# Optimization experiments

Measured on AMD Instinct MI355X. Metric: run time of the kernel, lower is better.

## Reference

```python
import jax, jax.numpy as jnp
import numpy as np

N_NODES = 40000
N_EDGES = 640000
IN_CH, HID_CH, OUT_CH = 128, 128, 64


def setup_inputs() -> dict:
    key = jax.random.key(0)
    ks = jax.random.split(key, 8)
    x = jax.random.normal(ks[0], (N_NODES, IN_CH), dtype=jnp.float32)
    edge_index = jax.random.randint(ks[1], (2, N_EDGES), 0, N_NODES, dtype=jnp.int32)
    s = 1.0 / np.sqrt(IN_CH)
    W1_rel = jax.random.normal(ks[2], (HID_CH, IN_CH), dtype=jnp.float32) * s
    W1_root = jax.random.normal(ks[3], (HID_CH, IN_CH), dtype=jnp.float32) * s
    b1 = jnp.zeros((HID_CH,), dtype=jnp.float32)
    s2 = 1.0 / np.sqrt(HID_CH)
    W2_rel = jax.random.normal(ks[4], (OUT_CH, HID_CH), dtype=jnp.float32) * s2
    W2_root = jax.random.normal(ks[5], (OUT_CH, HID_CH), dtype=jnp.float32) * s2
    b2 = jnp.zeros((OUT_CH,), dtype=jnp.float32)
    return {"x": x, "edge_index": edge_index, "W1_rel": W1_rel, "W1_root": W1_root,
            "b1": b1, "W2_rel": W2_rel, "W2_root": W2_root, "b2": b2}


def graph_conv(x, edge_index, W_rel, W_root, b):
    # PyG GraphConv (aggr='add'): out_i = W_rel @ (sum_{j->i} x_j) + W_root @ x_i + b
    src, dst = edge_index[0], edge_index[1]
    agg = jax.ops.segment_sum(x[src], dst, num_segments=x.shape[0])  # [N, d_in]
    return agg @ W_rel.T + x @ W_root.T + b


def reference(x, edge_index, W1_rel, W1_root, b1, W2_rel, W2_root, b2):
    h = jax.nn.relu(graph_conv(x, edge_index, W1_rel, W1_root, b1))
    return graph_conv(h, edge_index, W2_rel, W2_root, b2)
```

## Files before the change

### kernel.cpp

```cpp
#include <hip/hip_runtime.h>

#define N_NODES 40000
#define N_EDGES 640000

typedef __attribute__((ext_vector_type(8))) short short8;
typedef __attribute__((ext_vector_type(4))) float f32x4;

__device__ __forceinline__ float b2f_hi(uint v) {
  uint u = v & 0xffff0000u;
  return __builtin_bit_cast(float, u);
}
__device__ __forceinline__ float b2f_lo(uint v) {
  uint u = v << 16;
  return __builtin_bit_cast(float, u);
}
__device__ __forceinline__ ushort f2b(float f) {
  uint u = __builtin_bit_cast(uint, f);
  u += 0x7fffu + ((u >> 16) & 1u);
  return (ushort)(u >> 16);
}

__global__ __launch_bounds__(256) void k_count(
    const int* __restrict__ ei, int* __restrict__ deg) {
  int e = blockIdx.x * 256 + threadIdx.x;
  atomicAdd(&deg[ei[N_EDGES + e]], 1);
}

__global__ __launch_bounds__(256) void k_scanA(
    const int* __restrict__ deg, int* __restrict__ local,
    int* __restrict__ bsum) {
  const int t = threadIdx.x;
  const int base = blockIdx.x * 1024 + t * 4;
  int v0 = 0, v1 = 0, v2 = 0, v3 = 0;
  if (base < N_NODES) {
    int4 v = *reinterpret_cast<const int4*>(deg + base);
    v0 = v.x; v1 = v.y; v2 = v.z; v3 = v.w;
  }
  const int tot = v0 + v1 + v2 + v3;
  const int lane = t & 63;
  int ws = tot;
#pragma unroll
  for (int off = 1; off < 64; off <<= 1) {
    int y = __shfl_up(ws, off, 64);
    if (lane >= off) ws += y;
  }
  __shared__ int wsum[4];
  if (lane == 63) wsum[t >> 6] = ws;
  __syncthreads();
  const int w = t >> 6;
  int wbase = 0;
#pragma unroll
  for (int i = 0; i < 4; ++i) wbase += (i < w) ? wsum[i] : 0;
  const int incl = wbase + ws;
  const int excl = incl - tot;
  if (base < N_NODES) {
    int4 o;
    o.x = excl;
    o.y = excl + v0;
    o.z = excl + v0 + v1;
    o.w = excl + v0 + v1 + v2;
    *reinterpret_cast<int4*>(local + base) = o;
  }
  if (t == 255) bsum[blockIdx.x] = incl;
}

__global__ __launch_bounds__(64) void k_scanB(
    const int* __restrict__ bsum, int* __restrict__ bbase) {
  const int t = threadIdx.x;
  int v = (t < 40) ? bsum[t] : 0;
  int ws = v;
#pragma unroll
  for (int off = 1; off < 64; off <<= 1) {
    int y = __shfl_up(ws, off, 64);
    if (t >= off) ws += y;
  }
  if (t < 40) bbase[t] = ws - v;
}

__global__ __launch_bounds__(256) void k_scanC(
    const int* __restrict__ local, const int* __restrict__ bbase,
    int* __restrict__ offs, int* __restrict__ cursor) {
  int i = blockIdx.x * 256 + threadIdx.x;
  if (i < N_NODES) {
    int v = local[i] + bbase[i >> 10];
    offs[i] = v;
    cursor[i] = v;
  }
  if (i == 0) offs[N_NODES] = N_EDGES;
}

__global__ __launch_bounds__(256) void k_fill(
    const int* __restrict__ ei, int* __restrict__ cursor,
    int* __restrict__ csr_src) {
  int e = blockIdx.x * 256 + threadIdx.x;
  int dst = ei[N_EDGES + e];
  int idx = atomicAdd(&cursor[dst], 1);
  csr_src[idx] = ei[e];
}

__global__ __launch_bounds__(256) void k_cvt_x(
    const float* __restrict__ x, ushort* __restrict__ xb) {
  const int i = (blockIdx.x * 256 + threadIdx.x) * 8;
  float4 v0 = *reinterpret_cast<const float4*>(x + i);
  float4 v1 = *reinterpret_cast<const float4*>(x + i + 4);
  uint4 o;
  o.x = (uint)f2b(v0.x) | ((uint)f2b(v0.y) << 16);
  o.y = (uint)f2b(v0.z) | ((uint)f2b(v0.w) << 16);
  o.z = (uint)f2b(v1.x) | ((uint)f2b(v1.y) << 16);
  o.w = (uint)f2b(v1.z) | ((uint)f2b(v1.w) << 16);
  *reinterpret_cast<uint4*>(xb + i) = o;
}

__global__ __launch_bounds__(256) void k_cvt_w(
    const float* __restrict__ W1rel, const float* __restrict__ W1root,
    const float* __restrict__ W2rel, const float* __restrict__ W2root,
    ushort* __restrict__ Wb1, ushort* __restrict__ Wb2) {
  const int i = (blockIdx.x * 256 + threadIdx.x) * 4;
  const float* src;
  ushort* dst;
  if (i < 32768) {
    dst = Wb1 + i;
    src = (i < 16384) ? (W1rel + i) : (W1root + (i - 16384));
  } else {
    int j = i - 32768;
    dst = Wb2 + j;
    src = (j < 8192) ? (W2rel + j) : (W2root + (j - 8192));
  }
  float4 v = *reinterpret_cast<const float4*>(src);
  uint2 o;
  o.x = (uint)f2b(v.x) | ((uint)f2b(v.y) << 16);
  o.y = (uint)f2b(v.z) | ((uint)f2b(v.w) << 16);
  *reinterpret_cast<uint2*>(dst) = o;
}

template <int NCT, bool F32OUT1>
__global__ __launch_bounds__(256) void k_gemm_mfma(
    const ushort* __restrict__ A, const ushort* __restrict__ Wb,
    const float* __restrict__ bias, ushort* __restrict__ out0,
    void* __restrict__ out1v) {
  constexpr int HC = NCT * 8;
  const int t = threadIdx.x;
  const int lane = t & 63;
  const int n0 = blockIdx.x * 64 + (t >> 6) * 16;
  const int lr = lane & 15;
  const int hk = (lane >> 4) * 8;

  const ushort* arow = A + (size_t)(n0 + lr) * 128 + hk;
  const short8 a0 = *reinterpret_cast<const short8*>(arow);
  const short8 a1 = *reinterpret_cast<const short8*>(arow + 32);
  const short8 a2 = *reinterpret_cast<const short8*>(arow + 64);
  const short8 a3 = *reinterpret_cast<const short8*>(arow + 96);

  const int orow = n0 + (lane >> 4) * 4;

#pragma unroll
  for (int ct = 0; ct < NCT; ++ct) {
    const ushort* wrow = Wb + (size_t)(ct * 16 + lr) * 128 + hk;
    f32x4 acc = {0.f, 0.f, 0.f, 0.f};
    acc = __builtin_amdgcn_mfma_f32_16x16x32_bf16(
        a0, *reinterpret_cast<const short8*>(wrow), acc, 0, 0, 0);
    acc = __builtin_amdgcn_mfma_f32_16x16x32_bf16(
        a1, *reinterpret_cast<const short8*>(wrow + 32), acc, 0, 0, 0);
    acc = __builtin_amdgcn_mfma_f32_16x16x32_bf16(
        a2, *reinterpret_cast<const short8*>(wrow + 64), acc, 0, 0, 0);
    acc = __builtin_amdgcn_mfma_f32_16x16x32_bf16(
        a3, *reinterpret_cast<const short8*>(wrow + 96), acc, 0, 0, 0);

    if (ct < NCT / 2) {
      const int col = ct * 16 + lr;
#pragma unroll
      for (int i = 0; i < 4; ++i)
        out0[(size_t)(orow + i) * HC + col] = f2b(acc[i]);
    } else {
      const int col = (ct - NCT / 2) * 16 + lr;
      const float bb = bias[col];
      if (F32OUT1) {
        float* o1 = (float*)out1v;
#pragma unroll
        for (int i = 0; i < 4; ++i)
          o1[(size_t)(orow + i) * HC + col] = acc[i] + bb;
      } else {
        ushort* o1 = (ushort*)out1v;
#pragma unroll
        for (int i = 0; i < 4; ++i)
          o1[(size_t)(orow + i) * HC + col] = f2b(acc[i] + bb);
      }
    }
  }
}

__global__ __launch_bounds__(256) void k_gather_relu(
    const ushort* __restrict__ xr, ushort* __restrict__ h,
    const int* __restrict__ csr_src, const int* __restrict__ offs) {
  int n = blockIdx.x * 4 + (threadIdx.x >> 6);
  n = __builtin_amdgcn_readfirstlane(n);
  const int lane = threadIdx.x & 63;
  const int s = offs[n], e = offs[n + 1];
  float s00 = 0.f, s01 = 0.f, s10 = 0.f, s11 = 0.f;
  float s20 = 0.f, s21 = 0.f, s30 = 0.f, s31 = 0.f;
  int i = s;
  for (; i + 3 < e; i += 4) {
    int e0 = csr_src[i], e1 = csr_src[i + 1];
    int e2 = csr_src[i + 2], e3 = csr_src[i + 3];
    uint v0 = *reinterpret_cast<const uint*>(xr + (size_t)e0 * 128 + lane * 2);
    uint v1 = *reinterpret_cast<const uint*>(xr + (size_t)e1 * 128 + lane * 2);
    uint v2 = *reinterpret_cast<const uint*>(xr + (size_t)e2 * 128 + lane * 2);
    uint v3 = *reinterpret_cast<const uint*>(xr + (size_t)e3 * 128 + lane * 2);
    s00 += b2f_lo(v0); s01 += b2f_hi(v0);
    s10 += b2f_lo(v1); s11 += b2f_hi(v1);
    s20 += b2f_lo(v2); s21 += b2f_hi(v2);
    s30 += b2f_lo(v3); s31 += b2f_hi(v3);
  }
  for (; i < e; ++i) {
    uint v = *reinterpret_cast<const uint*>(
        xr + (size_t)csr_src[i] * 128 + lane * 2);
    s00 += b2f_lo(v); s01 += b2f_hi(v);
  }
  const float g0 = (s00 + s10) + (s20 + s30);
  const float g1 = (s01 + s11) + (s21 + s31);
  ushort* hp = h + (size_t)n * 128 + lane * 2;
  uint xov = *reinterpret_cast<const uint*>(hp);
  float r0 = fmaxf(b2f_lo(xov) + g0, 0.f);
  float r1 = fmaxf(b2f_hi(xov) + g1, 0.f);
  *reinterpret_cast<uint*>(hp) = (uint)f2b(r0) | ((uint)f2b(r1) << 16);
}

__global__ __launch_bounds__(256) void k_gather64(
    const ushort* __restrict__ t2, const int* __restrict__ csr_src,
    const int* __restrict__ offs, float* __restrict__ out) {
  int n = blockIdx.x * 4 + (threadIdx.x >> 6);
  n = __builtin_amdgcn_readfirstlane(n);
  const int lane = threadIdx.x & 63;
  const int s = offs[n], e = offs[n + 1];
  float a0 = 0.f, a1 = 0.f, a2 = 0.f, a3 = 0.f;
  int i = s;
  for (; i + 3 < e; i += 4) {
    int e0 = csr_src[i], e1 = csr_src[i + 1];
    int e2 = csr_src[i + 2], e3 = csr_src[i + 3];
    a0 += b2f_lo((uint)t2[(size_t)e0 * 64 + lane]);
    a1 += b2f_lo((uint)t2[(size_t)e1 * 64 + lane]);
    a2 += b2f_lo((uint)t2[(size_t)e2 * 64 + lane]);
    a3 += b2f_lo((uint)t2[(size_t)e3 * 64 + lane]);
  }
  for (; i < e; ++i)
    a0 += b2f_lo((uint)t2[(size_t)csr_src[i] * 64 + lane]);
  out[(size_t)n * 64 + lane] += (a0 + a1) + (a2 + a3);
}

extern "C" void kernel_launch(void* const* d_in, const int* in_sizes, int n_in,
                              void* d_out, int out_size, void* d_ws, size_t ws_size,
                              hipStream_t stream) {
  const float* x = (const float*)d_in[0];
  const int* ei = (const int*)d_in[1];
  const float* W1rel = (const float*)d_in[2];
  const float* W1root = (const float*)d_in[3];
  const float* b1 = (const float*)d_in[4];
  const float* W2rel = (const float*)d_in[5];
  const float* W2root = (const float*)d_in[6];
  const float* b2 = (const float*)d_in[7];
  float* out = (float*)d_out;

  ushort* xb = (ushort*)d_ws;
  ushort* xr = xb + (size_t)N_NODES * 128;
  ushort* xo = xr + (size_t)N_NODES * 128;
  ushort* t2 = xo + (size_t)N_NODES * 128;
  ushort* Wb1 = t2 + (size_t)N_NODES * 64;
  ushort* Wb2 = Wb1 + 32768;
  int* deg = (int*)(Wb2 + 16384);
  int* offs = deg + N_NODES;
  int* cursor = offs + (N_NODES + 1);
  int* csr_src = cursor + N_NODES;
  int* bsum = csr_src + N_EDGES;
  int* bbase = bsum + 64;
  int* local = (int*)xr;

  k_cvt_x<<<(N_NODES * 128 / 8) / 256, 256, 0, stream>>>(x, xb);
  k_cvt_w<<<48, 256, 0, stream>>>(W1rel, W1root, W2rel, W2root, Wb1, Wb2);

  hipMemsetAsync(deg, 0, (size_t)N_NODES * sizeof(int), stream);
  k_count<<<N_EDGES / 256, 256, 0, stream>>>(ei, deg);
  k_scanA<<<(N_NODES + 1023) / 1024, 256, 0, stream>>>(deg, local, bsum);
  k_scanB<<<1, 64, 0, stream>>>(bsum, bbase);
  k_scanC<<<(N_NODES + 255) / 256, 256, 0, stream>>>(local, bbase, offs, cursor);
  k_fill<<<N_EDGES / 256, 256, 0, stream>>>(ei, cursor, csr_src);

  k_gemm_mfma<16, false><<<N_NODES / 64, 256, 0, stream>>>(
      xb, Wb1, b1, xr, (void*)xo);
  k_gather_relu<<<N_NODES / 4, 256, 0, stream>>>(xr, xo, csr_src, offs);

  k_gemm_mfma<8, true><<<N_NODES / 64, 256, 0, stream>>>(
      xo, Wb2, b2, t2, (void*)out);
  k_gather64<<<N_NODES / 4, 256, 0, stream>>>(t2, csr_src, offs, out);
}
```

Baseline: 240.2 us.

## Fuse layer-1 gather/ReLU into layer-2 GEMM and fold x conversion into GEMM1

```diff
diff --git a/kernel.cpp b/kernel.cpp
--- a/kernel.cpp
+++ b/kernel.cpp
@@ -18,6 +18,35 @@
   uint u = __builtin_bit_cast(uint, f);
   u += 0x7fffu + ((u >> 16) & 1u);
   return (ushort)(u >> 16);
+}
+
+__global__ __launch_bounds__(256) void k_prep(
+    const float* __restrict__ W1rel, const float* __restrict__ W1root,
+    const float* __restrict__ W2rel, const float* __restrict__ W2root,
+    ushort* __restrict__ Wb1, ushort* __restrict__ Wb2,
+    int* __restrict__ deg) {
+  const int b = blockIdx.x;
+  if (b < 48) {
+    const int i = (b * 256 + threadIdx.x) * 4;
+    const float* src;
+    ushort* dst;
+    if (i < 32768) {
+      dst = Wb1 + i;
+      src = (i < 16384) ? (W1rel + i) : (W1root + (i - 16384));
+    } else {
+      int j = i - 32768;
+      dst = Wb2 + j;
+      src = (j < 8192) ? (W2rel + j) : (W2root + (j - 8192));
+    }
+    float4 v = *reinterpret_cast<const float4*>(src);
+    uint2 o;
+    o.x = (uint)f2b(v.x) | ((uint)f2b(v.y) << 16);
+    o.y = (uint)f2b(v.z) | ((uint)f2b(v.w) << 16);
+    *reinterpret_cast<uint2*>(dst) = o;
+  } else {
+    const int i = (b - 48) * 256 + threadIdx.x;
+    if (i < N_NODES) deg[i] = 0;
+  }
 }
 
 __global__ __launch_bounds__(256) void k_count(
@@ -98,66 +127,117 @@
   csr_src[idx] = ei[e];
 }
 
-__global__ __launch_bounds__(256) void k_cvt_x(
-    const float* __restrict__ x, ushort* __restrict__ xb) {
-  const int i = (blockIdx.x * 256 + threadIdx.x) * 8;
-  float4 v0 = *reinterpret_cast<const float4*>(x + i);
-  float4 v1 = *reinterpret_cast<const float4*>(x + i + 4);
-  uint4 o;
-  o.x = (uint)f2b(v0.x) | ((uint)f2b(v0.y) << 16);
-  o.y = (uint)f2b(v0.z) | ((uint)f2b(v0.w) << 16);
-  o.z = (uint)f2b(v1.x) | ((uint)f2b(v1.y) << 16);
-  o.w = (uint)f2b(v1.z) | ((uint)f2b(v1.w) << 16);
-  *reinterpret_cast<uint4*>(xb + i) = o;
-}
-
-__global__ __launch_bounds__(256) void k_cvt_w(
-    const float* __restrict__ W1rel, const float* __restrict__ W1root,
-    const float* __restrict__ W2rel, const float* __restrict__ W2root,
-    ushort* __restrict__ Wb1, ushort* __restrict__ Wb2) {
-  const int i = (blockIdx.x * 256 + threadIdx.x) * 4;
-  const float* src;
-  ushort* dst;
-  if (i < 32768) {
-    dst = Wb1 + i;
-    src = (i < 16384) ? (W1rel + i) : (W1root + (i - 16384));
-  } else {
-    int j = i - 32768;
-    dst = Wb2 + j;
-    src = (j < 8192) ? (W2rel + j) : (W2root + (j - 8192));
-  }
-  float4 v = *reinterpret_cast<const float4*>(src);
-  uint2 o;
-  o.x = (uint)f2b(v.x) | ((uint)f2b(v.y) << 16);
-  o.y = (uint)f2b(v.z) | ((uint)f2b(v.w) << 16);
-  *reinterpret_cast<uint2*>(dst) = o;
-}
-
-template <int NCT, bool F32OUT1>
-__global__ __launch_bounds__(256) void k_gemm_mfma(
-    const ushort* __restrict__ A, const ushort* __restrict__ Wb,
-    const float* __restrict__ bias, ushort* __restrict__ out0,
-    void* __restrict__ out1v) {
-  constexpr int HC = NCT * 8;
+__global__ __launch_bounds__(256) void k_gemm1_mfma(
+    const float* __restrict__ x, const ushort* __restrict__ Wb1,
+    const float* __restrict__ b1, ushort* __restrict__ xr,
+    ushort* __restrict__ xo) {
   const int t = threadIdx.x;
   const int lane = t & 63;
   const int n0 = blockIdx.x * 64 + (t >> 6) * 16;
   const int lr = lane & 15;
   const int hk = (lane >> 4) * 8;
 
-  const ushort* arow = A + (size_t)(n0 + lr) * 128 + hk;
-  const short8 a0 = *reinterpret_cast<const short8*>(arow);
-  const short8 a1 = *reinterpret_cast<const short8*>(arow + 32);
-  const short8 a2 = *reinterpret_cast<const short8*>(arow + 64);
-  const short8 a3 = *reinterpret_cast<const short8*>(arow + 96);
+  const float* arow = x + (size_t)(n0 + lr) * 128 + hk;
+  short8 a[4];
+#pragma unroll
+  for (int c = 0; c < 4; ++c) {
+    float4 f0 = *reinterpret_cast<const float4*>(arow + c * 32);
+    float4 f1 = *reinterpret_cast<const float4*>(arow + c * 32 + 4);
+    short8 v;
+    v[0] = (short)f2b(f0.x); v[1] = (short)f2b(f0.y);
+    v[2] = (short)f2b(f0.z); v[3] = (short)f2b(f0.w);
+    v[4] = (short)f2b(f1.x); v[5] = (short)f2b(f1.y);
+    v[6] = (short)f2b(f1.z); v[7] = (short)f2b(f1.w);
+    a[c] = v;
+  }
 
   const int orow = n0 + (lane >> 4) * 4;
 
 #pragma unroll
-  for (int ct = 0; ct < NCT; ++ct) {
-    const ushort* wrow = Wb + (size_t)(ct * 16 + lr) * 128 + hk;
+  for (int ct = 0; ct < 16; ++ct) {
+    const ushort* wrow = Wb1 + (size_t)(ct * 16 + lr) * 128 + hk;
     f32x4 acc = {0.f, 0.f, 0.f, 0.f};
     acc = __builtin_amdgcn_mfma_f32_16x16x32_bf16(
+        a[0], *reinterpret_cast<const short8*>(wrow), acc, 0, 0, 0);
+    acc = __builtin_amdgcn_mfma_f32_16x16x32_bf16(
+        a[1], *reinterpret_cast<const short8*>(wrow + 32), acc, 0, 0, 0);
+    acc = __builtin_amdgcn_mfma_f32_16x16x32_bf16(
+        a[2], *reinterpret_cast<const short8*>(wrow + 64), acc, 0, 0, 0);
+    acc = __builtin_amdgcn_mfma_f32_16x16x32_bf16(
+        a[3], *reinterpret_cast<const short8*>(wrow + 96), acc, 0, 0, 0);
+
+    if (ct < 8) {
+      const int col = ct * 16 + lr;
+#pragma unroll
+      for (int i = 0; i < 4; ++i)
+        xr[(size_t)(orow + i) * 128 + col] = f2b(acc[i]);
+    } else {
+      const int col = (ct - 8) * 16 + lr;
+      const float bb = b1[col];
+#pragma unroll
+      for (int i = 0; i < 4; ++i)
+        xo[(size_t)(orow + i) * 128 + col] = f2b(acc[i] + bb);
+    }
+  }
+}
+
+__global__ __launch_bounds__(256) void k_gemm2_fused(
+    const ushort* __restrict__ xr, const ushort* __restrict__ xo,
+    const ushort* __restrict__ Wb2, const float* __restrict__ b2,
+    const int* __restrict__ csr_src, const int* __restrict__ offs,
+    ushort* __restrict__ t2, float* __restrict__ out) {
+  __shared__ ushort sH[64][136];
+  const int t = threadIdx.x;
+  const int wave = t >> 6;
+  const int lane = t & 63;
+  const int nb = blockIdx.x * 64 + wave * 16;
+
+  for (int r = 0; r < 16; ++r) {
+    const int n = nb + r;
+    const int s = offs[n], e = offs[n + 1];
+    float s00 = 0.f, s01 = 0.f, s10 = 0.f, s11 = 0.f;
+    float s20 = 0.f, s21 = 0.f, s30 = 0.f, s31 = 0.f;
+    int i = s;
+    for (; i + 3 < e; i += 4) {
+      int e0 = csr_src[i], e1 = csr_src[i + 1];
+      int e2 = csr_src[i + 2], e3 = csr_src[i + 3];
+      uint v0 = *reinterpret_cast<const uint*>(xr + (size_t)e0 * 128 + lane * 2);
+      uint v1 = *reinterpret_cast<const uint*>(xr + (size_t)e1 * 128 + lane * 2);
+      uint v2 = *reinterpret_cast<const uint*>(xr + (size_t)e2 * 128 + lane * 2);
+      uint v3 = *reinterpret_cast<const uint*>(xr + (size_t)e3 * 128 + lane * 2);
+      s00 += b2f_lo(v0); s01 += b2f_hi(v0);
+      s10 += b2f_lo(v1); s11 += b2f_hi(v1);
+      s20 += b2f_lo(v2); s21 += b2f_hi(v2);
+      s30 += b2f_lo(v3); s31 += b2f_hi(v3);
+    }
+    for (; i < e; ++i) {
+      uint v = *reinterpret_cast<const uint*>(
+          xr + (size_t)csr_src[i] * 128 + lane * 2);
+      s00 += b2f_lo(v); s01 += b2f_hi(v);
+    }
+    uint xov = *reinterpret_cast<const uint*>(xo + (size_t)n * 128 + lane * 2);
+    float r0 = fmaxf(b2f_lo(xov) + ((s00 + s10) + (s20 + s30)), 0.f);
+    float r1 = fmaxf(b2f_hi(xov) + ((s01 + s11) + (s21 + s31)), 0.f);
+    *reinterpret_cast<uint*>(&sH[wave * 16 + r][lane * 2]) =
+        (uint)f2b(r0) | ((uint)f2b(r1) << 16);
+  }
+  __syncthreads();
+
+  const int lr = lane & 15;
+  const int hk = (lane >> 4) * 8;
+  const ushort* hrow = &sH[wave * 16 + lr][0];
+  const short8 a0 = *reinterpret_cast<const short8*>(hrow + hk);
+  const short8 a1 = *reinterpret_cast<const short8*>(hrow + 32 + hk);
+  const short8 a2 = *reinterpret_cast<const short8*>(hrow + 64 + hk);
+  const short8 a3 = *reinterpret_cast<const short8*>(hrow + 96 + hk);
+
+  const int orow = nb + (lane >> 4) * 4;
+
+#pragma unroll
+  for (int ct = 0; ct < 8; ++ct) {
+    const ushort* wrow = Wb2 + (size_t)(ct * 16 + lr) * 128 + hk;
+    f32x4 acc = {0.f, 0.f, 0.f, 0.f};
+    acc = __builtin_amdgcn_mfma_f32_16x16x32_bf16(
         a0, *reinterpret_cast<const short8*>(wrow), acc, 0, 0, 0);
     acc = __builtin_amdgcn_mfma_f32_16x16x32_bf16(
         a1, *reinterpret_cast<const short8*>(wrow + 32), acc, 0, 0, 0);
@@ -166,63 +246,19 @@
     acc = __builtin_amdgcn_mfma_f32_16x16x32_bf16(
         a3, *reinterpret_cast<const short8*>(wrow + 96), acc, 0, 0, 0);
 
-    if (ct < NCT / 2) {
+    if (ct < 4) {
       const int col = ct * 16 + lr;
 #pragma unroll
       for (int i = 0; i < 4; ++i)
-        out0[(size_t)(orow + i) * HC + col] = f2b(acc[i]);
+        t2[(size_t)(orow + i) * 64 + col] = f2b(acc[i]);
     } else {
-      const int col = (ct - NCT / 2) * 16 + lr;
-      const float bb = bias[col];
-      if (F32OUT1) {
-        float* o1 = (float*)out1v;
-#pragma unroll
-        for (int i = 0; i < 4; ++i)
-          o1[(size_t)(orow + i) * HC + col] = acc[i] + bb;
-      } else {
-        ushort* o1 = (ushort*)out1v;
-#pragma unroll
-        for (int i = 0; i < 4; ++i)
-          o1[(size_t)(orow + i) * HC + col] = f2b(acc[i] + bb);
-      }
-    }
-  }
-}
-
-__global__ __launch_bounds__(256) void k_gather_relu(
-    const ushort* __restrict__ xr, ushort* __restrict__ h,
-    const int* __restrict__ csr_src, const int* __restrict__ offs) {
-  int n = blockIdx.x * 4 + (threadIdx.x >> 6);
-  n = __builtin_amdgcn_readfirstlane(n);
-  const int lane = threadIdx.x & 63;
-  const int s = offs[n], e = offs[n + 1];
-  float s00 = 0.f, s01 = 0.f, s10 = 0.f, s11 = 0.f;
-  float s20 = 0.f, s21 = 0.f, s30 = 0.f, s31 = 0.f;
-  int i = s;
-  for (; i + 3 < e; i += 4) {
-    int e0 = csr_src[i], e1 = csr_src[i + 1];
-    int e2 = csr_src[i + 2], e3 = csr_src[i + 3];
-    uint v0 = *reinterpret_cast<const uint*>(xr + (size_t)e0 * 128 + lane * 2);
-    uint v1 = *reinterpret_cast<const uint*>(xr + (size_t)e1 * 128 + lane * 2);
-    uint v2 = *reinterpret_cast<const uint*>(xr + (size_t)e2 * 128 + lane * 2);
-    uint v3 = *reinterpret_cast<const uint*>(xr + (size_t)e3 * 128 + lane * 2);
-    s00 += b2f_lo(v0); s01 += b2f_hi(v0);
-    s10 += b2f_lo(v1); s11 += b2f_hi(v1);
-    s20 += b2f_lo(v2); s21 += b2f_hi(v2);
-    s30 += b2f_lo(v3); s31 += b2f_hi(v3);
-  }
-  for (; i < e; ++i) {
-    uint v = *reinterpret_cast<const uint*>(
-        xr + (size_t)csr_src[i] * 128 + lane * 2);
-    s00 += b2f_lo(v); s01 += b2f_hi(v);
-  }
-  const float g0 = (s00 + s10) + (s20 + s30);
-  const float g1 = (s01 + s11) + (s21 + s31);
-  ushort* hp = h + (size_t)n * 128 + lane * 2;
-  uint xov = *reinterpret_cast<const uint*>(hp);
-  float r0 = fmaxf(b2f_lo(xov) + g0, 0.f);
-  float r1 = fmaxf(b2f_hi(xov) + g1, 0.f);
-  *reinterpret_cast<uint*>(hp) = (uint)f2b(r0) | ((uint)f2b(r1) << 16);
+      const int col = (ct - 4) * 16 + lr;
+      const float bb = b2[col];
+#pragma unroll
+      for (int i = 0; i < 4; ++i)
+        out[(size_t)(orow + i) * 64 + col] = acc[i] + bb;
+    }
+  }
 }
 
 __global__ __launch_bounds__(256) void k_gather64(
@@ -260,8 +296,7 @@
   const float* b2 = (const float*)d_in[7];
   float* out = (float*)d_out;
 
-  ushort* xb = (ushort*)d_ws;
-  ushort* xr = xb + (size_t)N_NODES * 128;
+  ushort* xr = (ushort*)d_ws;
   ushort* xo = xr + (size_t)N_NODES * 128;
   ushort* t2 = xo + (size_t)N_NODES * 128;
   ushort* Wb1 = t2 + (size_t)N_NODES * 64;
@@ -274,21 +309,18 @@
   int* bbase = bsum + 64;
   int* local = (int*)xr;
 
-  k_cvt_x<<<(N_NODES * 128 / 8) / 256, 256, 0, stream>>>(x, xb);
-  k_cvt_w<<<48, 256, 0, stream>>>(W1rel, W1root, W2rel, W2root, Wb1, Wb2);
-
-  hipMemsetAsync(deg, 0, (size_t)N_NODES * sizeof(int), stream);
+  k_prep<<<205, 256, 0, stream>>>(W1rel, W1root, W2rel, W2root, Wb1, Wb2, deg);
+
   k_count<<<N_EDGES / 256, 256, 0, stream>>>(ei, deg);
   k_scanA<<<(N_NODES + 1023) / 1024, 256, 0, stream>>>(deg, local, bsum);
   k_scanB<<<1, 64, 0, stream>>>(bsum, bbase);
   k_scanC<<<(N_NODES + 255) / 256, 256, 0, stream>>>(local, bbase, offs, cursor);
   k_fill<<<N_EDGES / 256, 256, 0, stream>>>(ei, cursor, csr_src);
 
-  k_gemm_mfma<16, false><<<N_NODES / 64, 256, 0, stream>>>(
-      xb, Wb1, b1, xr, (void*)xo);
-  k_gather_relu<<<N_NODES / 4, 256, 0, stream>>>(xr, xo, csr_src, offs);
-
-  k_gemm_mfma<8, true><<<N_NODES / 64, 256, 0, stream>>>(
-      xo, Wb2, b2, t2, (void*)out);
+  k_gemm1_mfma<<<N_NODES / 64, 256, 0, stream>>>(x, Wb1, b1, xr, xo);
+
+  k_gemm2_fused<<<N_NODES / 64, 256, 0, stream>>>(
+      xr, xo, Wb2, b2, csr_src, offs, t2, out);
+
   k_gather64<<<N_NODES / 4, 256, 0, stream>>>(t2, csr_src, offs, out);
 }
```

Result: slower. 275.6 us (+14.7%).
